# Kernel tuning notes

Hardware: AMD Instinct MI355X
Metric: run time of the kernel (lower is better)

Reference implementation:

```python
import jax, jax.numpy as jnp
import numpy as np

B, D, H = 16384, 1024, 4096


def setup_inputs() -> dict:
    key = jax.random.key(0)
    kx, kp, k1, k2 = jax.random.split(key, 4)
    X = jax.random.normal(kx, (B, D), dtype=jnp.float32)
    prot_col_idx = 3
    # protected column must be binary {0,1} so the remap produces no NaNs
    prot = jax.random.randint(kp, (B,), 0, 2).astype(jnp.float32)
    X = X.at[:, prot_col_idx].set(prot)
    W1 = jax.random.normal(k1, (D, H), dtype=jnp.float32) * (1.0 / np.sqrt(D))
    b1 = jnp.zeros((H,), dtype=jnp.float32)
    W2 = jax.random.normal(k2, (H, D), dtype=jnp.float32) * (1.0 / np.sqrt(H))
    b2 = jnp.zeros((D,), dtype=jnp.float32)
    return {"X": X, "W1": W1, "b1": b1, "W2": W2, "b2": b2,
            "prot_col_idx": prot_col_idx}


def reference(X, W1, b1, W2, b2, prot_col_idx):
    def explainer(x):
        h = jnp.tanh(x @ W1 + b1)          # [B, H]
        return h @ W2 + b2                  # [B, D]

    # vectorized remap of the protected column: 0 -> 1, 1 -> 0, else NaN
    col = X[:, prot_col_idx]
    flipped = jnp.where(col == 0, jnp.float32(1.0),
                        jnp.where(col == 1, jnp.float32(0.0), jnp.float32(jnp.nan)))
    X_copy = X.at[:, prot_col_idx].set(flipped.astype(X.dtype))

    shaps = explainer(X)
    shaps_counter = explainer(X_copy)
    mean_euclid_dist = jnp.mean(jnp.abs(shaps - shaps_counter), axis=0)  # [D]
    return mean_euclid_dist.sum()
```

## Files before the change

### kernel.cpp

```cpp
#include <hip/hip_runtime.h>
#include <stdint.h>

#define B_N 16384
#define D_N 1024
#define H_N 4096

typedef int i32x4 __attribute__((ext_vector_type(4)));
typedef int i32x8 __attribute__((ext_vector_type(8)));
typedef float f32x4 __attribute__((ext_vector_type(4)));

__device__ __forceinline__ void gload16(const void* g, void* l) {
  __builtin_amdgcn_global_load_lds((const __attribute__((address_space(1))) void*)g,
                                   (__attribute__((address_space(3))) void*)l,
                                   16, 0, 0);
}

__device__ __forceinline__ unsigned char f2fp8(float v) {
  return (unsigned char)(__builtin_amdgcn_cvt_pk_fp8_f32(v, v, 0, false) & 0xFF);
}

__device__ __forceinline__ int perm_h(int h) {
  return (h & ~63) | ((h & 15) << 2) | ((h >> 4) & 3);
}

__global__ __launch_bounds__(256) void pack_x_kernel(
    const float4* __restrict__ X4, int* __restrict__ Xb,
    float* __restrict__ s, const int* __restrict__ pci_p,
    float* __restrict__ out0) {
  int i = (blockIdx.x * 256 + threadIdx.x) * 2;
  if (blockIdx.x == 0 && threadIdx.x == 0) out0[0] = 0.0f;
  int pci = *pci_p;
#pragma unroll
  for (int u = 0; u < 2; u++) {
    float4 v = X4[i + u];
    int p = __builtin_amdgcn_cvt_pk_fp8_f32(v.x, v.y, 0, false);
    p = __builtin_amdgcn_cvt_pk_fp8_f32(v.z, v.w, p, true);
    Xb[i + u] = p;
    if (((i + u) & (D_N / 4 - 1)) == (pci >> 2)) {
      int row = (i + u) >> 8;
      float c;
      switch (pci & 3) {
        case 0:  c = v.x; break;
        case 1:  c = v.y; break;
        case 2:  c = v.z; break;
        default: c = v.w; break;
      }
      s[row] = 1.0f - 2.0f * c;
    }
  }
}

__device__ __forceinline__ void transpose_tile(
    const float* __restrict__ in, unsigned char* __restrict__ out,
    int R, int C, float scale, float* __restrict__ w3, int pci,
    int i0, int j0, int tx, int ty, bool permute) {
  __shared__ float tile[32][33];
#pragma unroll
  for (int r = 0; r < 32; r += 8) {
    int i = i0 + ty + r;
    int j = j0 + tx;
    float v = in[(size_t)i * C + j];
    tile[ty + r][tx] = v;
    if (w3 != nullptr && i == pci) w3[j] = v;
  }
  __syncthreads();
#pragma unroll
  for (int r = 0; r < 32; r += 8) {
    int jo = j0 + ty + r;
    int io = i0 + tx;
    int ioo = permute ? perm_h(io) : io;
    out[(size_t)jo * R + ioo] = f2fp8(tile[tx][ty + r] * scale);
  }
}

__global__ __launch_bounds__(256) void transpose_kernel(
    const float* __restrict__ W1, unsigned char* __restrict__ W1T, float* __restrict__ w3,
    const float* __restrict__ W2, unsigned char* __restrict__ W2T,
    const int* __restrict__ pci_p) {
  int b = blockIdx.x;
  int tid = threadIdx.x;
  int pci = *pci_p;
  if (b < 4096) {
    transpose_tile(W1, W1T, D_N, H_N, 16.0f, w3, pci,
                   (b >> 7) * 32, (b & 127) * 32, tid & 31, tid >> 5, false);
  } else {
    int id = b - 4096;
    transpose_tile(W2, W2T, H_N, D_N, 64.0f, nullptr, -1,
                   (id >> 5) * 32, (id & 31) * 32, tid & 31, tid >> 5, true);
  }
}

template <int KTOT>
__device__ __forceinline__ void mx_mainloop(
    const unsigned char* __restrict__ A, const unsigned char* __restrict__ B,
    int m0, int n0, int sa, int sb,
    unsigned char* As, unsigned char* Bs, f32x4 (&acc)[4][4]) {
  const int tid = threadIdx.x;
  const int lane = tid & 63;
  const int wave = tid >> 6;
  const int wm = (wave >> 1) * 64;
  const int wn = (wave & 1) * 64;
  const int lm = lane & 15;
  const int quad = lane >> 4;

  const int srow = tid >> 3;
  const int clog = (tid & 7) ^ (srow & 7);
  const unsigned char* Ag = A + (size_t)(m0 + srow) * KTOT + clog * 16;
  const unsigned char* Bg = B + (size_t)(n0 + srow) * KTOT + clog * 16;
  unsigned char* As_l = As + tid * 16;
  unsigned char* Bs_l = Bs + tid * 16;

  for (int k0 = 0; k0 < KTOT; k0 += 128) {
#pragma unroll
    for (int it = 0; it < 4; it++) {
      gload16(Ag + k0 + (size_t)(32 * it) * KTOT, As_l + it * 4096);
      gload16(Bg + k0 + (size_t)(32 * it) * KTOT, Bs_l + it * 4096);
    }
    __syncthreads();
    i32x8 a[4], b[4];
#pragma unroll
    for (int i = 0; i < 4; i++) {
      int r = wm + i * 16 + lm;
      int e = r & 7;
      i32x4 lo = *(const i32x4*)&As[r * 128 + ((2 * quad) ^ e) * 16];
      i32x4 hi = *(const i32x4*)&As[r * 128 + ((2 * quad + 1) ^ e) * 16];
      a[i] = __builtin_shufflevector(lo, hi, 0, 1, 2, 3, 4, 5, 6, 7);
    }
#pragma unroll
    for (int j = 0; j < 4; j++) {
      int r = wn + j * 16 + lm;
      int e = r & 7;
      i32x4 lo = *(const i32x4*)&Bs[r * 128 + ((2 * quad) ^ e) * 16];
      i32x4 hi = *(const i32x4*)&Bs[r * 128 + ((2 * quad + 1) ^ e) * 16];
      b[j] = __builtin_shufflevector(lo, hi, 0, 1, 2, 3, 4, 5, 6, 7);
    }
#pragma unroll
    for (int i = 0; i < 4; i++)
#pragma unroll
      for (int j = 0; j < 4; j++)
        acc[i][j] = __builtin_amdgcn_mfma_scale_f32_16x16x128_f8f6f4(
            a[i], b[j], acc[i][j], 0, 0, 0, sa, 0, sb);
    __syncthreads();
  }
}

__global__ __launch_bounds__(256) void gemm1_dh(
    const unsigned char* __restrict__ Xb,
    const unsigned char* __restrict__ W1T,
    const float* __restrict__ b1,
    const float* __restrict__ w3,
    const float* __restrict__ s,
    unsigned int* __restrict__ Dh4) {
  __shared__ alignas(16) unsigned char As[128 * 128];
  __shared__ alignas(16) unsigned char Bs[128 * 128];
  int l = blockIdx.y * gridDim.x + blockIdx.x;
  int x = l & 7;
  int k = l >> 3;
  int ni = k & 7;
  int m  = (k >> 3) & 15;
  int nc = k >> 7;
  const int m0 = (x * 16 + m) * 128;
  const int n0 = (nc * 8 + ni) * 128;

  f32x4 acc[4][4] = {};
  mx_mainloop<D_N>(Xb, W1T, m0, n0, 127, 123, As, Bs, acc);

  const int tid = threadIdx.x;
  const int lane = tid & 63;
  const int wave = tid >> 6;
  const int wm = (wave >> 1) * 64;
  const int wn = (wave & 1) * 64;
  const int lm = lane & 15;
  const int quad = lane >> 4;

  float ewp[4], ewm[4], nump[4], numm[4], b1v[4];
#pragma unroll
  for (int j = 0; j < 4; j++) {
    int gh = n0 + wn + j * 16 + lm;
    float w = w3[gh];
    float ep = __expf(2.0f * w);
    float em = __expf(-2.0f * w);
    ewp[j] = ep; ewm[j] = em;
    nump[j] = 128.0f * (1.0f - ep);
    numm[j] = 128.0f * (1.0f - em);
    b1v[j] = b1[gh];
  }
  const size_t coloff = (size_t)((n0 + wn) >> 2) + lm;
#pragma unroll
  for (int i = 0; i < 4; i++) {
#pragma unroll
    for (int r = 0; r < 4; r++) {
      int gb = m0 + wm + i * 16 + quad * 4 + r;
      bool sp = s[gb] > 0.0f;
      float o[4];
#pragma unroll
      for (int j = 0; j < 4; j++) {
        float ews = sp ? ewp[j] : ewm[j];
        float num = sp ? nump[j] : numm[j];
        float z = fminf(acc[i][j][r] + b1v[j], 12.0f);
        float E = __expf(2.0f * z);
        float den = (E * ews + 1.0f) * (E + 1.0f);
        o[j] = (E * num) * __builtin_amdgcn_rcpf(den);
      }
      int p = __builtin_amdgcn_cvt_pk_fp8_f32(o[0], o[1], 0, false);
      p = __builtin_amdgcn_cvt_pk_fp8_f32(o[2], o[3], p, true);
      Dh4[(size_t)gb * (H_N / 4) + coloff] = (unsigned int)p;
    }
  }
}

__global__ __launch_bounds__(256) void gemm2_abs(
    const unsigned char* __restrict__ Dh,
    const unsigned char* __restrict__ W2T,
    float* __restrict__ out) {
  __shared__ alignas(16) unsigned char As[128 * 128];
  __shared__ alignas(16) unsigned char Bs[128 * 128];
  __shared__ float wsum[4];
  int l = blockIdx.y * gridDim.x + blockIdx.x;
  int x = l & 7;
  int k = l >> 3;
  int c = k >> 6;
  int idx = k & 63;
  int m  = idx >> 2;
  int nj = idx & 3;
  const int m0 = (x * 16 + m) * 128;
  const int n0 = (c * 4 + nj) * 128;

  f32x4 acc[4][4] = {};
  mx_mainloop<H_N>(Dh, W2T, m0, n0, 121, 121, As, Bs, acc);

  const int tid = threadIdx.x;
  const int lane = tid & 63;
  const int wave = tid >> 6;

  float t = 0.0f;
#pragma unroll
  for (int i = 0; i < 4; i++)
#pragma unroll
    for (int j = 0; j < 4; j++)
#pragma unroll
      for (int r = 0; r < 4; r++)
        t += fabsf(acc[i][j][r]);

#pragma unroll
  for (int off2 = 32; off2 > 0; off2 >>= 1)
    t += __shfl_down(t, off2, 64);
  if (lane == 0) wsum[wave] = t;
  __syncthreads();
  if (tid == 0)
    atomicAdd(out, (wsum[0] + wsum[1] + wsum[2] + wsum[3]) * (1.0f / (float)B_N));
}

extern "C" void kernel_launch(void* const* d_in, const int* in_sizes, int n_in,
                              void* d_out, int out_size, void* d_ws, size_t ws_size,
                              hipStream_t stream) {
  const float* X  = (const float*)d_in[0];
  const float* W1 = (const float*)d_in[1];
  const float* b1 = (const float*)d_in[2];
  const float* W2 = (const float*)d_in[3];
  const int* pci  = (const int*)d_in[5];

  char* ws = (char*)d_ws;
  size_t off = 0;
  unsigned char* Xb  = (unsigned char*)(ws + off); off += (size_t)B_N * D_N;
  unsigned char* W1T = (unsigned char*)(ws + off); off += (size_t)H_N * D_N;
  unsigned char* W2T = (unsigned char*)(ws + off); off += (size_t)D_N * H_N;
  float* w3  = (float*)(ws + off); off += (size_t)H_N * 4;
  float* s   = (float*)(ws + off); off += (size_t)B_N * 4;
  unsigned char* Dh  = (unsigned char*)(ws + off); off += (size_t)B_N * H_N;
  if (ws_size < off) return;

  pack_x_kernel<<<8192, 256, 0, stream>>>((const float4*)X, (int*)Xb, s, pci,
                                          (float*)d_out);
  transpose_kernel<<<8192, 256, 0, stream>>>(W1, W1T, w3, W2, W2T, pci);
  gemm1_dh<<<dim3(32, 128), 256, 0, stream>>>(Xb, W1T, b1, w3, s,
                                              (unsigned int*)Dh);
  gemm2_abs<<<dim3(8, 128), 256, 0, stream>>>(Dh, W2T, (float*)d_out);
}
```

Measured before the change: 309.0 us.

## Merge prep kernels, stream A-fragment loads, and raise GEMM occupancy bounds

```diff
diff --git a/kernel.cpp b/kernel.cpp
--- a/kernel.cpp
+++ b/kernel.cpp
@@ -21,33 +21,6 @@
 
 __device__ __forceinline__ int perm_h(int h) {
   return (h & ~63) | ((h & 15) << 2) | ((h >> 4) & 3);
-}
-
-__global__ __launch_bounds__(256) void pack_x_kernel(
-    const float4* __restrict__ X4, int* __restrict__ Xb,
-    float* __restrict__ s, const int* __restrict__ pci_p,
-    float* __restrict__ out0) {
-  int i = (blockIdx.x * 256 + threadIdx.x) * 2;
-  if (blockIdx.x == 0 && threadIdx.x == 0) out0[0] = 0.0f;
-  int pci = *pci_p;
-#pragma unroll
-  for (int u = 0; u < 2; u++) {
-    float4 v = X4[i + u];
-    int p = __builtin_amdgcn_cvt_pk_fp8_f32(v.x, v.y, 0, false);
-    p = __builtin_amdgcn_cvt_pk_fp8_f32(v.z, v.w, p, true);
-    Xb[i + u] = p;
-    if (((i + u) & (D_N / 4 - 1)) == (pci >> 2)) {
-      int row = (i + u) >> 8;
-      float c;
-      switch (pci & 3) {
-        case 0:  c = v.x; break;
-        case 1:  c = v.y; break;
-        case 2:  c = v.z; break;
-        default: c = v.w; break;
-      }
-      s[row] = 1.0f - 2.0f * c;
-    }
-  }
 }
 
 __device__ __forceinline__ void transpose_tile(
@@ -73,18 +46,42 @@
   }
 }
 
-__global__ __launch_bounds__(256) void transpose_kernel(
+__global__ __launch_bounds__(256) void prep_kernel(
+    const float4* __restrict__ X4, int* __restrict__ Xb,
+    float* __restrict__ s,
     const float* __restrict__ W1, unsigned char* __restrict__ W1T, float* __restrict__ w3,
     const float* __restrict__ W2, unsigned char* __restrict__ W2T,
-    const int* __restrict__ pci_p) {
+    const int* __restrict__ pci_p, float* __restrict__ out0) {
   int b = blockIdx.x;
   int tid = threadIdx.x;
   int pci = *pci_p;
-  if (b < 4096) {
+  if (b == 0 && tid == 0) out0[0] = 0.0f;
+  if (b < 8192) {
+    int i = (b * 256 + tid) * 2;
+#pragma unroll
+    for (int u = 0; u < 2; u++) {
+      float4 v = X4[i + u];
+      int p = __builtin_amdgcn_cvt_pk_fp8_f32(v.x, v.y, 0, false);
+      p = __builtin_amdgcn_cvt_pk_fp8_f32(v.z, v.w, p, true);
+      Xb[i + u] = p;
+      if (((i + u) & (D_N / 4 - 1)) == (pci >> 2)) {
+        int row = (i + u) >> 8;
+        float c;
+        switch (pci & 3) {
+          case 0:  c = v.x; break;
+          case 1:  c = v.y; break;
+          case 2:  c = v.z; break;
+          default: c = v.w; break;
+        }
+        s[row] = 1.0f - 2.0f * c;
+      }
+    }
+  } else if (b < 12288) {
+    int id = b - 8192;
     transpose_tile(W1, W1T, D_N, H_N, 16.0f, w3, pci,
-                   (b >> 7) * 32, (b & 127) * 32, tid & 31, tid >> 5, false);
+                   (id >> 7) * 32, (id & 127) * 32, tid & 31, tid >> 5, false);
   } else {
-    int id = b - 4096;
+    int id = b - 12288;
     transpose_tile(W2, W2T, H_N, D_N, 64.0f, nullptr, -1,
                    (id >> 5) * 32, (id & 31) * 32, tid & 31, tid >> 5, true);
   }
@@ -117,15 +114,7 @@
       gload16(Bg + k0 + (size_t)(32 * it) * KTOT, Bs_l + it * 4096);
     }
     __syncthreads();
-    i32x8 a[4], b[4];
-#pragma unroll
-    for (int i = 0; i < 4; i++) {
-      int r = wm + i * 16 + lm;
-      int e = r & 7;
-      i32x4 lo = *(const i32x4*)&As[r * 128 + ((2 * quad) ^ e) * 16];
-      i32x4 hi = *(const i32x4*)&As[r * 128 + ((2 * quad + 1) ^ e) * 16];
-      a[i] = __builtin_shufflevector(lo, hi, 0, 1, 2, 3, 4, 5, 6, 7);
-    }
+    i32x8 b[4];
 #pragma unroll
     for (int j = 0; j < 4; j++) {
       int r = wn + j * 16 + lm;
@@ -135,16 +124,22 @@
       b[j] = __builtin_shufflevector(lo, hi, 0, 1, 2, 3, 4, 5, 6, 7);
     }
 #pragma unroll
-    for (int i = 0; i < 4; i++)
+    for (int i = 0; i < 4; i++) {
+      int r = wm + i * 16 + lm;
+      int e = r & 7;
+      i32x4 lo = *(const i32x4*)&As[r * 128 + ((2 * quad) ^ e) * 16];
+      i32x4 hi = *(const i32x4*)&As[r * 128 + ((2 * quad + 1) ^ e) * 16];
+      i32x8 av = __builtin_shufflevector(lo, hi, 0, 1, 2, 3, 4, 5, 6, 7);
 #pragma unroll
       for (int j = 0; j < 4; j++)
         acc[i][j] = __builtin_amdgcn_mfma_scale_f32_16x16x128_f8f6f4(
-            a[i], b[j], acc[i][j], 0, 0, 0, sa, 0, sb);
+            av, b[j], acc[i][j], 0, 0, 0, sa, 0, sb);
+    }
     __syncthreads();
   }
 }
 
-__global__ __launch_bounds__(256) void gemm1_dh(
+__global__ __launch_bounds__(256, 4) void gemm1_dh(
     const unsigned char* __restrict__ Xb,
     const unsigned char* __restrict__ W1T,
     const float* __restrict__ b1,
@@ -209,7 +204,7 @@
   }
 }
 
-__global__ __launch_bounds__(256) void gemm2_abs(
+__global__ __launch_bounds__(256, 4) void gemm2_abs(
     const unsigned char* __restrict__ Dh,
     const unsigned char* __restrict__ W2T,
     float* __restrict__ out) {
@@ -270,9 +265,9 @@
   unsigned char* Dh  = (unsigned char*)(ws + off); off += (size_t)B_N * H_N;
   if (ws_size < off) return;
 
-  pack_x_kernel<<<8192, 256, 0, stream>>>((const float4*)X, (int*)Xb, s, pci,
-                                          (float*)d_out);
-  transpose_kernel<<<8192, 256, 0, stream>>>(W1, W1T, w3, W2, W2T, pci);
+  prep_kernel<<<16384, 256, 0, stream>>>((const float4*)X, (int*)Xb, s,
+                                         W1, W1T, w3, W2, W2T, pci,
+                                         (float*)d_out);
   gemm1_dh<<<dim3(32, 128), 256, 0, stream>>>(Xb, W1T, b1, w3, s,
                                               (unsigned int*)Dh);
   gemm2_abs<<<dim3(8, 128), 256, 0, stream>>>(Dh, W2T, (float*)d_out);
```

Result: faster. 283.4 us (-8.3%).
